# Kernel tuning notes

Hardware: AMD Instinct MI355X
Metric: run time of the kernel (lower is better)

The kernel has to match this reference:

```python
import jax, jax.numpy as jnp
import numpy as np

B, S, E, F = 8, 2048, 1024, 4096
EPS = 1e-5


def _layer_norm(x, gamma, beta):
    mu = jnp.mean(x, axis=-1, keepdims=True)
    var = jnp.mean((x - mu) ** 2, axis=-1, keepdims=True)
    return (x - mu) * jax.lax.rsqrt(var + EPS) * gamma + beta


def setup_inputs() -> dict:
    key = jax.random.key(0)
    ks = jax.random.split(key, 16)
    s = 0.02
    return {
        "x": jax.random.normal(ks[0], (B, S, E), dtype=jnp.float32),
        "Wq": jax.random.normal(ks[1], (E, E), dtype=jnp.float32) * s,
        "bq": jnp.zeros((E,), dtype=jnp.float32),
        "Wk": jax.random.normal(ks[2], (E, E), dtype=jnp.float32) * s,
        "bk": jnp.zeros((E,), dtype=jnp.float32),
        "Wv": jax.random.normal(ks[3], (E, E), dtype=jnp.float32) * s,
        "bv": jnp.zeros((E,), dtype=jnp.float32),
        "gamma1": jnp.ones((E,), dtype=jnp.float32),
        "beta1": jnp.zeros((E,), dtype=jnp.float32),
        "W1": jax.random.normal(ks[4], (E, F), dtype=jnp.float32) * s,
        "b1": jnp.zeros((F,), dtype=jnp.float32),
        "W2": jax.random.normal(ks[5], (F, E), dtype=jnp.float32) * s,
        "b2": jnp.zeros((E,), dtype=jnp.float32),
        "gamma2": jnp.ones((E,), dtype=jnp.float32),
        "beta2": jnp.zeros((E,), dtype=jnp.float32),
    }


def reference(x, Wq, bq, Wk, bk, Wv, bv, gamma1, beta1, W1, b1, W2, b2, gamma2, beta2):
    # Single-head attention exactly as the torch forward (neurogenesis=False path).
    q = x @ Wq + bq  # [B,S,E]
    k = x @ Wk + bk
    v = x @ Wv + bv
    scores = jnp.einsum('bse,bte->bst', q, k) / jnp.sqrt(jnp.float32(E))
    attn = jax.nn.softmax(scores, axis=-1)
    attn_out = jnp.einsum('bst,bte->bse', attn, v)
    # dropout is identity in eval mode
    h = _layer_norm(x + attn_out, gamma1, beta1)
    ffn = jax.nn.relu(h @ W1 + b1) @ W2 + b2
    out = _layer_norm(h + ffn, gamma2, beta2)
    return (out, k, q, v)
```

## Files before the change

kernel.cpp:

```cpp
#include <hip/hip_runtime.h>
#include <hip/hip_bf16.h>
#include <stdint.h>

typedef __attribute__((ext_vector_type(8))) short s16x8;
typedef __attribute__((ext_vector_type(4))) float f32x4;

static constexpr int Bb = 8, Ss = 2048, Ee = 1024, Ff = 4096;
static constexpr int M_TOK = Bb * Ss;
static constexpr size_t OUT_SLOT = (size_t)M_TOK * Ee;

__device__ inline unsigned short f2bf(float f) {
  unsigned int u = __float_as_uint(f);
  unsigned int r = (u + 0x7FFFu + ((u >> 16) & 1u)) >> 16;
  return (unsigned short)r;
}
__device__ inline float bf2f(unsigned short h) {
  return __uint_as_float(((unsigned int)h) << 16);
}

__device__ inline void gload16(const unsigned short* g, const unsigned short* l) {
  __builtin_amdgcn_global_load_lds(
      (const __attribute__((address_space(1))) void*)g,
      (__attribute__((address_space(3))) void*)(unsigned short*)l, 16, 0, 0);
}

__global__ __launch_bounds__(256) void k_cvt_f32_bf16(const float* __restrict__ in,
                                                      unsigned short* __restrict__ out, int n4) {
  int i = blockIdx.x * blockDim.x + threadIdx.x;
  int stride = gridDim.x * blockDim.x;
  for (; i < n4; i += stride) {
    float4 v = ((const float4*)in)[i];
    ushort4 o;
    o.x = f2bf(v.x); o.y = f2bf(v.y); o.z = f2bf(v.z); o.w = f2bf(v.w);
    ((ushort4*)out)[i] = o;
  }
}

__global__ __launch_bounds__(256) void k_transpose_w(const float* __restrict__ in,
                                                     unsigned short* __restrict__ out,
                                                     int R, int C) {
  __shared__ float t[32][33];
  int c0 = blockIdx.x * 32, r0 = blockIdx.y * 32;
  int tx = threadIdx.x, ty = threadIdx.y;
  for (int i = ty; i < 32; i += 8)
    t[i][tx] = in[(size_t)(r0 + i) * C + c0 + tx];
  __syncthreads();
  for (int i = ty; i < 32; i += 8)
    out[(size_t)(c0 + i) * R + r0 + tx] = f2bf(t[tx][i]);
}

__global__ __launch_bounds__(256) void k_transpose_v(const unsigned short* __restrict__ v,
                                                     unsigned short* __restrict__ vT) {
  __shared__ unsigned short t[32][33];
  int b = blockIdx.z;
  const unsigned short* in = v + (size_t)b * Ss * Ee;
  unsigned short* out = vT + (size_t)b * Ee * Ss;
  int c0 = blockIdx.x * 32, r0 = blockIdx.y * 32;
  int tx = threadIdx.x, ty = threadIdx.y;
  for (int i = ty; i < 32; i += 8)
    t[i][tx] = in[(size_t)(r0 + i) * Ee + c0 + tx];
  __syncthreads();
  for (int i = ty; i < 32; i += 8)
    out[(size_t)(c0 + i) * Ss + r0 + tx] = t[tx][i];
}

template <bool WF32, bool WB16, bool RELU, bool HAS_BIAS>
__global__ __launch_bounds__(512, 2) void k_gemm256(const unsigned short* __restrict__ A,
                                                    const unsigned short* __restrict__ Bt,
                                                    float* __restrict__ Cf,
                                                    unsigned short* __restrict__ Cb,
                                                    const float* __restrict__ bias,
                                                    int M, int N, int K,
                                                    long aBatch, long bBatch, long cBatch,
                                                    float scale) {
  __shared__ unsigned short lds[4][2][256 * 32];
  const int tid = threadIdx.x;
  const int lane = tid & 63;
  const int wid = tid >> 6;
  const int wr = wid >> 2, wc = wid & 3;

  const int gx = gridDim.x;
  const int nwg = gx * gridDim.y;
  const int id = blockIdx.y * gx + blockIdx.x;
  const int qq = nwg >> 3;
  const int sid = (id & 7) * qq + (id >> 3);
  const int m0 = (sid % gx) * 256, n0 = (sid / gx) * 256;
  const int z = blockIdx.z;
  A += (size_t)z * aBatch;
  Bt += (size_t)z * bBatch;

  const int srow = tid >> 2;
  const int csrc = (tid & 3) ^ (srow & 3);
  const unsigned short* ga0 = A + (size_t)(m0 + srow) * K + csrc * 8;
  const unsigned short* ga1 = A + (size_t)(m0 + 128 + srow) * K + csrc * 8;
  const unsigned short* gb0 = Bt + (size_t)(n0 + srow) * K + csrc * 8;
  const unsigned short* gb1 = Bt + (size_t)(n0 + 128 + srow) * K + csrc * 8;
  const int waveDst = (wid << 9);

  auto STAGE = [&](int step) {
    const int slot = step & 3;
    const size_t ko = (size_t)step << 5;
    const unsigned short* la = &lds[slot][0][0];
    const unsigned short* lb = &lds[slot][1][0];
    gload16(ga0 + ko, la + waveDst);
    gload16(ga1 + ko, la + 4096 + waveDst);
    gload16(gb0 + ko, lb + waveDst);
    gload16(gb1 + ko, lb + 4096 + waveDst);
  };

  f32x4 acc[8][4] = {};
  const int fr = lane & 15;
  const int cc = ((lane >> 4) ^ (fr & 3)) * 8;
  const int nt = K >> 5;

  STAGE(0); STAGE(1); STAGE(2);

  for (int t = 0; t < nt; ++t) {
    if (t + 3 < nt) {
      STAGE(t + 3);
      asm volatile("s_waitcnt vmcnt(12)" ::: "memory");
    } else {
      const int rem = nt - 1 - t;
      if (rem == 2)      asm volatile("s_waitcnt vmcnt(8)" ::: "memory");
      else if (rem == 1) asm volatile("s_waitcnt vmcnt(4)" ::: "memory");
      else               asm volatile("s_waitcnt vmcnt(0)" ::: "memory");
    }
    __builtin_amdgcn_s_barrier();
    asm volatile("" ::: "memory");

    const int slot = t & 3;
    const unsigned short* la = &lds[slot][0][0];
    const unsigned short* lb = &lds[slot][1][0];
    __builtin_amdgcn_s_setprio(1);
    s16x8 bf[4];
#pragma unroll
    for (int ni = 0; ni < 4; ++ni)
      bf[ni] = *(const s16x8*)(lb + ((wc * 64 + ni * 16 + fr) * 32 + cc));
#pragma unroll
    for (int mi = 0; mi < 8; ++mi) {
      s16x8 af = *(const s16x8*)(la + ((wr * 128 + mi * 16 + fr) * 32 + cc));
#pragma unroll
      for (int ni = 0; ni < 4; ++ni)
        acc[mi][ni] = __builtin_amdgcn_mfma_f32_16x16x32_bf16(af, bf[ni], acc[mi][ni], 0, 0, 0);
    }
    __builtin_amdgcn_s_setprio(0);
    asm volatile("" ::: "memory");
    __builtin_amdgcn_s_barrier();
  }

  const int er = lane & 15, eq = lane >> 4;
#pragma unroll
  for (int mi = 0; mi < 8; ++mi) {
#pragma unroll
    for (int ni = 0; ni < 4; ++ni) {
#pragma unroll
      for (int r = 0; r < 4; ++r) {
        int row = m0 + wr * 128 + mi * 16 + eq * 4 + r;
        int col = n0 + wc * 64 + ni * 16 + er;
        float v = acc[mi][ni][r] * scale;
        if (HAS_BIAS) v += bias[col];
        if (RELU) v = v > 0.f ? v : 0.f;
        size_t idx = (size_t)z * cBatch + (size_t)row * N + col;
        if (WF32) Cf[idx] = v;
        if (WB16) Cb[idx] = f2bf(v);
      }
    }
  }
}

__global__ __launch_bounds__(256) void k_softmax(unsigned short* __restrict__ sa) {
  __shared__ float red[4];
  const int row = blockIdx.x;
  const int tid = threadIdx.x;
  unsigned short* sr = sa + (size_t)row * Ss;
  ushort4 u0 = ((const ushort4*)sr)[tid];
  ushort4 u1 = ((const ushort4*)sr)[tid + 256];
  float e[8];
  e[0] = bf2f(u0.x); e[1] = bf2f(u0.y); e[2] = bf2f(u0.z); e[3] = bf2f(u0.w);
  e[4] = bf2f(u1.x); e[5] = bf2f(u1.y); e[6] = bf2f(u1.z); e[7] = bf2f(u1.w);
  float m = fmaxf(fmaxf(fmaxf(e[0], e[1]), fmaxf(e[2], e[3])),
                  fmaxf(fmaxf(e[4], e[5]), fmaxf(e[6], e[7])));
  for (int s = 1; s < 64; s <<= 1) m = fmaxf(m, __shfl_xor(m, s, 64));
  if ((tid & 63) == 0) red[tid >> 6] = m;
  __syncthreads();
  m = fmaxf(fmaxf(red[0], red[1]), fmaxf(red[2], red[3]));
  __syncthreads();
  float sum = 0.f;
#pragma unroll
  for (int j = 0; j < 8; ++j) { e[j] = __expf(e[j] - m); sum += e[j]; }
  for (int s = 1; s < 64; s <<= 1) sum += __shfl_xor(sum, s, 64);
  if ((tid & 63) == 0) red[tid >> 6] = sum;
  __syncthreads();
  sum = red[0] + red[1] + red[2] + red[3];
  float inv = 1.f / sum;
  ushort4 o0, o1;
  o0.x = f2bf(e[0] * inv); o0.y = f2bf(e[1] * inv);
  o0.z = f2bf(e[2] * inv); o0.w = f2bf(e[3] * inv);
  o1.x = f2bf(e[4] * inv); o1.y = f2bf(e[5] * inv);
  o1.z = f2bf(e[6] * inv); o1.w = f2bf(e[7] * inv);
  ((ushort4*)sr)[tid] = o0;
  ((ushort4*)sr)[tid + 256] = o1;
}

template <bool A_F32, bool OUT_F32>
__global__ __launch_bounds__(256) void k_ln(const void* __restrict__ a,
                                            const unsigned short* __restrict__ bb,
                                            const float* __restrict__ gamma,
                                            const float* __restrict__ beta,
                                            void* __restrict__ outp) {
  __shared__ float red[4];
  const int row = blockIdx.x;
  const int tid = threadIdx.x;
  float v[4];
  if (A_F32) {
    float4 av = ((const float4*)((const float*)a + (size_t)row * Ee))[tid];
    v[0] = av.x; v[1] = av.y; v[2] = av.z; v[3] = av.w;
  } else {
    ushort4 av = ((const ushort4*)((const unsigned short*)a + (size_t)row * Ee))[tid];
    v[0] = bf2f(av.x); v[1] = bf2f(av.y); v[2] = bf2f(av.z); v[3] = bf2f(av.w);
  }
  ushort4 bv = ((const ushort4*)(bb + (size_t)row * Ee))[tid];
  v[0] += bf2f(bv.x); v[1] += bf2f(bv.y); v[2] += bf2f(bv.z); v[3] += bf2f(bv.w);
  float s = v[0] + v[1] + v[2] + v[3];
  float q = v[0] * v[0] + v[1] * v[1] + v[2] * v[2] + v[3] * v[3];
  for (int sh = 1; sh < 64; sh <<= 1) {
    s += __shfl_xor(s, sh, 64);
    q += __shfl_xor(q, sh, 64);
  }
  if ((tid & 63) == 0) red[tid >> 6] = s;
  __syncthreads();
  s = red[0] + red[1] + red[2] + red[3];
  __syncthreads();
  if ((tid & 63) == 0) red[tid >> 6] = q;
  __syncthreads();
  q = red[0] + red[1] + red[2] + red[3];
  float mu = s * (1.f / Ee);
  float var = q * (1.f / Ee) - mu * mu;
  float rinv = rsqrtf(var + 1e-5f);
  int c = tid * 4;
  float o0 = (v[0] - mu) * rinv * gamma[c + 0] + beta[c + 0];
  float o1 = (v[1] - mu) * rinv * gamma[c + 1] + beta[c + 1];
  float o2 = (v[2] - mu) * rinv * gamma[c + 2] + beta[c + 2];
  float o3 = (v[3] - mu) * rinv * gamma[c + 3] + beta[c + 3];
  if (OUT_F32) {
    float4 o; o.x = o0; o.y = o1; o.z = o2; o.w = o3;
    ((float4*)((float*)outp + (size_t)row * Ee))[tid] = o;
  } else {
    ushort4 o;
    o.x = f2bf(o0); o.y = f2bf(o1); o.z = f2bf(o2); o.w = f2bf(o3);
    ((ushort4*)((unsigned short*)outp + (size_t)row * Ee))[tid] = o;
  }
}

extern "C" void kernel_launch(void* const* d_in, const int* in_sizes, int n_in,
                              void* d_out, int out_size, void* d_ws, size_t ws_size,
                              hipStream_t stream) {
  const float* x = (const float*)d_in[0];
  const float* Wq = (const float*)d_in[1];
  const float* bq = (const float*)d_in[2];
  const float* Wk = (const float*)d_in[3];
  const float* bk = (const float*)d_in[4];
  const float* Wv = (const float*)d_in[5];
  const float* bv = (const float*)d_in[6];
  const float* g1 = (const float*)d_in[7];
  const float* be1 = (const float*)d_in[8];
  const float* W1 = (const float*)d_in[9];
  const float* b1 = (const float*)d_in[10];
  const float* W2 = (const float*)d_in[11];
  const float* b2 = (const float*)d_in[12];
  const float* g2 = (const float*)d_in[13];
  const float* be2 = (const float*)d_in[14];

  float* out = (float*)d_out;
  float* kO = out + OUT_SLOT;
  float* qO = out + 2 * OUT_SLOT;
  float* vO = out + 3 * OUT_SLOT;

  char* ws = (char*)d_ws;
  unsigned short* xb  = (unsigned short*)(ws + 0);
  unsigned short* WqT = (unsigned short*)(ws + 33554432ull);
  unsigned short* WkT = (unsigned short*)(ws + 35651584ull);
  unsigned short* WvT = (unsigned short*)(ws + 37748736ull);
  unsigned short* W1T = (unsigned short*)(ws + 39845888ull);
  unsigned short* W2T = (unsigned short*)(ws + 48234496ull);
  unsigned short* qb  = (unsigned short*)(ws + 56623104ull);
  unsigned short* kb  = (unsigned short*)(ws + 90177536ull);
  unsigned short* vb  = (unsigned short*)(ws + 123731968ull);
  unsigned short* scb = (unsigned short*)(ws + 157286400ull);
  unsigned short* vT  = (unsigned short*)(ws + 224395264ull);
  unsigned short* ao  = (unsigned short*)(ws + 56623104ull);
  unsigned short* hb  = (unsigned short*)(ws + 90177536ull);
  unsigned short* f1b = (unsigned short*)(ws + 157286400ull);
  unsigned short* f2b = (unsigned short*)(ws + 123731968ull);

  dim3 tb(32, 8);
  k_cvt_f32_bf16<<<2048, 256, 0, stream>>>(x, xb, M_TOK * Ee / 4);
  k_transpose_w<<<dim3(32, 32), tb, 0, stream>>>(Wq, WqT, Ee, Ee);
  k_transpose_w<<<dim3(32, 32), tb, 0, stream>>>(Wk, WkT, Ee, Ee);
  k_transpose_w<<<dim3(32, 32), tb, 0, stream>>>(Wv, WvT, Ee, Ee);
  k_transpose_w<<<dim3(128, 32), tb, 0, stream>>>(W1, W1T, Ee, Ff);
  k_transpose_w<<<dim3(32, 128), tb, 0, stream>>>(W2, W2T, Ff, Ee);
  k_gemm256<true, true, false, true><<<dim3(64, 4, 1), 512, 0, stream>>>(
      xb, WqT, qO, qb, bq, M_TOK, Ee, Ee, 0, 0, 0, 1.f);
  k_gemm256<true, true, false, true><<<dim3(64, 4, 1), 512, 0, stream>>>(
      xb, WkT, kO, kb, bk, M_TOK, Ee, Ee, 0, 0, 0, 1.f);
  k_gemm256<true, true, false, true><<<dim3(64, 4, 1), 512, 0, stream>>>(
      xb, WvT, vO, vb, bv, M_TOK, Ee, Ee, 0, 0, 0, 1.f);
  k_gemm256<false, true, false, false><<<dim3(8, 8, 8), 512, 0, stream>>>(
      qb, kb, nullptr, scb, nullptr, Ss, Ss, Ee, (long)Ss * Ee, (long)Ss * Ee, (long)Ss * Ss,
      0.03125f);
  k_softmax<<<Bb * Ss, 256, 0, stream>>>(scb);
  k_transpose_v<<<dim3(32, 64, 8), tb, 0, stream>>>(vb, vT);
  k_gemm256<false, true, false, false><<<dim3(8, 4, 8), 512, 0, stream>>>(
      scb, vT, nullptr, ao, nullptr, Ss, Ee, Ss, (long)Ss * Ss, (long)Ee * Ss, (long)Ss * Ee, 1.f);
  k_ln<true, false><<<M_TOK, 256, 0, stream>>>(x, ao, g1, be1, hb);
  k_gemm256<false, true, true, true><<<dim3(64, 16, 1), 512, 0, stream>>>(
      hb, W1T, nullptr, f1b, b1, M_TOK, Ff, Ee, 0, 0, 0, 1.f);
  k_gemm256<false, true, false, true><<<dim3(64, 4, 1), 512, 0, stream>>>(
      f1b, W2T, nullptr, f2b, b2, M_TOK, Ee, Ff, 0, 0, 0, 1.f);
  k_ln<false, true><<<M_TOK, 256, 0, stream>>>(hb, f2b, g2, be2, out);
}
```

Baseline: 798.7 us.

## Double-buffer B fragments in registers and regroup GEMM tile swizzle into 4-row groups

The GEMM main loop is unrolled by two and ping-pongs the B-operand LDS fragments between two register sets. The next step's B reads are issued before the barrier so they overlap the current step's MFMAs, and the vmcnt waits are retuned to the new issue order. The tile-to-workgroup mapping now groups four M-tiles per column stripe to improve L2 reuse of the B operand. Register pressure rises from the extra fragment buffers under launch_bounds(512,2). The loop also assumes an even K-step count and a correct wait count.

```diff
diff --git a/kernel.cpp b/kernel.cpp
--- a/kernel.cpp
+++ b/kernel.cpp
@@ -79,12 +79,15 @@
   const int wid = tid >> 6;
   const int wr = wid >> 2, wc = wid & 3;
 
-  const int gx = gridDim.x;
-  const int nwg = gx * gridDim.y;
+  const int gx = gridDim.x, gy = gridDim.y;
+  const int nwg = gx * gy;
   const int id = blockIdx.y * gx + blockIdx.x;
   const int qq = nwg >> 3;
-  const int sid = (id & 7) * qq + (id >> 3);
-  const int m0 = (sid % gx) * 256, n0 = (sid / gx) * 256;
+  const int s = (id & 7) * qq + (id >> 3);
+  const int g4 = s / (gy * 4);
+  const int r4 = s - g4 * gy * 4;
+  const int m0 = (g4 * 4 + (r4 & 3)) * 256;
+  const int n0 = (r4 >> 2) * 256;
   const int z = blockIdx.z;
   A += (size_t)z * aBatch;
   Bt += (size_t)z * bBatch;
@@ -113,37 +116,56 @@
   const int cc = ((lane >> 4) ^ (fr & 3)) * 8;
   const int nt = K >> 5;
 
+  auto RD_B = [&](int slot, s16x8* rb) {
+    const unsigned short* lb = &lds[slot][1][0];
+#pragma unroll
+    for (int ni = 0; ni < 4; ++ni)
+      rb[ni] = *(const s16x8*)(lb + ((wc * 64 + ni * 16 + fr) * 32 + cc));
+  };
+  auto PHASE_MM = [&](int slot, s16x8* rb) {
+    const unsigned short* la = &lds[slot][0][0];
+    __builtin_amdgcn_s_setprio(1);
+    s16x8 ra[8];
+#pragma unroll
+    for (int mi = 0; mi < 8; ++mi)
+      ra[mi] = *(const s16x8*)(la + ((wr * 128 + mi * 16 + fr) * 32 + cc));
+#pragma unroll
+    for (int mi = 0; mi < 8; ++mi)
+#pragma unroll
+      for (int ni = 0; ni < 4; ++ni)
+        acc[mi][ni] = __builtin_amdgcn_mfma_f32_16x16x32_bf16(ra[mi], rb[ni], acc[mi][ni], 0, 0, 0);
+    __builtin_amdgcn_s_setprio(0);
+  };
+  auto VMW = [&](int p) {
+    const int rem = nt - p;
+    if (rem > 3)      asm volatile("s_waitcnt vmcnt(8)" ::: "memory");
+    else if (rem == 3) asm volatile("s_waitcnt vmcnt(4)" ::: "memory");
+    else               asm volatile("s_waitcnt vmcnt(0)" ::: "memory");
+  };
+
+  s16x8 BA[4], BB[4];
+
   STAGE(0); STAGE(1); STAGE(2);
-
-  for (int t = 0; t < nt; ++t) {
-    if (t + 3 < nt) {
-      STAGE(t + 3);
-      asm volatile("s_waitcnt vmcnt(12)" ::: "memory");
-    } else {
-      const int rem = nt - 1 - t;
-      if (rem == 2)      asm volatile("s_waitcnt vmcnt(8)" ::: "memory");
-      else if (rem == 1) asm volatile("s_waitcnt vmcnt(4)" ::: "memory");
-      else               asm volatile("s_waitcnt vmcnt(0)" ::: "memory");
-    }
+  asm volatile("s_waitcnt vmcnt(4)" ::: "memory");
+  __builtin_amdgcn_s_barrier();
+  asm volatile("" ::: "memory");
+  RD_B(0, BA);
+
+  for (int t = 0; t < nt; t += 2) {
+    RD_B((t + 1) & 3, BB);
+    if (t + 3 < nt) STAGE(t + 3);
+    VMW(t);
     __builtin_amdgcn_s_barrier();
     asm volatile("" ::: "memory");
-
-    const int slot = t & 3;
-    const unsigned short* la = &lds[slot][0][0];
-    const unsigned short* lb = &lds[slot][1][0];
-    __builtin_amdgcn_s_setprio(1);
-    s16x8 bf[4];
-#pragma unroll
-    for (int ni = 0; ni < 4; ++ni)
-      bf[ni] = *(const s16x8*)(lb + ((wc * 64 + ni * 16 + fr) * 32 + cc));
-#pragma unroll
-    for (int mi = 0; mi < 8; ++mi) {
-      s16x8 af = *(const s16x8*)(la + ((wr * 128 + mi * 16 + fr) * 32 + cc));
-#pragma unroll
-      for (int ni = 0; ni < 4; ++ni)
-        acc[mi][ni] = __builtin_amdgcn_mfma_f32_16x16x32_bf16(af, bf[ni], acc[mi][ni], 0, 0, 0);
-    }
-    __builtin_amdgcn_s_setprio(0);
+    PHASE_MM(t & 3, BA);
+    asm volatile("" ::: "memory");
+    __builtin_amdgcn_s_barrier();
+    if (t + 2 < nt) RD_B((t + 2) & 3, BA);
+    if (t + 4 < nt) STAGE(t + 4);
+    VMW(t + 1);
+    __builtin_amdgcn_s_barrier();
+    asm volatile("" ::: "memory");
+    PHASE_MM((t + 1) & 3, BB);
     asm volatile("" ::: "memory");
     __builtin_amdgcn_s_barrier();
   }
```

Result: faster. 735.5 us (-7.9%).
